# Kernel tuning notes

Hardware: AMD Instinct MI355X
Metric: run time of the kernel (lower is better)

## Reference

```python
import jax, jax.numpy as jnp
import numpy as np

N_NODES = 100000
N_EDGES = 2400000


def setup_inputs() -> dict:
    key = jax.random.key(0)
    ks = jax.random.split(key, 8)
    x = jax.random.normal(ks[0], (N_NODES, 1), dtype=jnp.float32)
    edge_index = jax.random.randint(ks[1], (2, N_EDGES), 0, N_NODES, dtype=jnp.int64)
    # GCNConv weights: lin (in, out) and bias (out,), glorot-ish init
    def w(k, fan_in, fan_out):
        return jax.random.normal(k, (fan_in, fan_out), dtype=jnp.float32) / np.sqrt(fan_in)
    return {
        "x": x,
        "edge_index": edge_index,
        "W1": w(ks[2], 1, 32), "b1": jnp.zeros((32,), jnp.float32),
        "W2": w(ks[3], 32, 16), "b2": jnp.zeros((16,), jnp.float32),
        "W3": w(ks[4], 16, 1), "b3": jnp.zeros((1,), jnp.float32),
    }


def _gcn_conv(x, W, b, src, dst, norm, n):
    # x: [N, Fin] -> linear first (cheaper), then gather-scale-scatter
    h = x @ W                                   # [N, Fout]
    msg = h[src] * norm[:, None]                # [E+N, Fout] gather on src
    out = jax.ops.segment_sum(msg, dst, num_segments=n)  # scatter-add on dst
    return out + b


def reference(x, edge_index, W1, b1, W2, b2, W3, b3):
    n = x.shape[0]
    loops = jnp.arange(n, dtype=edge_index.dtype)
    src = jnp.concatenate([edge_index[0], loops])  # PyG: add self-loops
    dst = jnp.concatenate([edge_index[1], loops])
    # symmetric normalization: deg computed on targets with unit edge weights
    deg = jax.ops.segment_sum(jnp.ones_like(src, dtype=x.dtype), dst, num_segments=n)
    dis = jnp.where(deg > 0, jax.lax.rsqrt(deg), 0.0)
    norm = dis[src] * dis[dst]                  # [E+N]
    h = jax.nn.relu(_gcn_conv(x, W1, b1, src, dst, norm, n))
    h = jax.nn.relu(_gcn_conv(h, W2, b2, src, dst, norm, n))
    return _gcn_conv(h, W3, b3, src, dst, norm, n)
```

## Files before the change

kernel.cpp:

```cpp
#include <hip/hip_runtime.h>
#include <hip/hip_fp16.h>

static constexpr int NN   = 100000;
static constexpr int NE   = 2400000;
static constexpr int BSH  = 7;
static constexpr int BSZ  = 128;
static constexpr int NB   = (NN + BSZ - 1) / BSZ;
static constexpr int MSH  = 9;
static constexpr unsigned MMSK = 511;
static constexpr int MBN  = (NN + 511) / 512;
static constexpr int CAPM = 13184;
static constexpr int NPB  = 512;
static constexpr int SEG  = 4688;
static constexpr int CAP  = 4224;
static_assert((size_t)NPB * SEG >= NE, "segments cover edge list");
static_assert(MBN <= 256, "mid hist fits one pass");
static_assert(NN % 16 == 0, "16-lane-per-node kernels assume NN % 16 == 0");

__global__ __launch_bounds__(256) void khistM(const int* __restrict__ dst,
                                              unsigned* __restrict__ H) {
    __shared__ unsigned h[MBN];
    int b = blockIdx.x, t = threadIdx.x;
    for (int k = t; k < MBN; k += 256) h[k] = 0;
    __syncthreads();
    int off = b * SEG;
    int n = NE - off; if (n > SEG) n = SEG;
    for (int j = t; j < n; j += 256)
        atomicAdd(&h[(unsigned)dst[off + j] >> MSH], 1u);
    __syncthreads();
    for (int k = t; k < MBN; k += 256) H[(size_t)b * MBN + k] = h[k];
}

__global__ __launch_bounds__(512) void kscanM(const unsigned* __restrict__ H,
                                              unsigned* __restrict__ P,
                                              unsigned* __restrict__ cntM) {
    __shared__ unsigned a[512], b2[512];
    int k = blockIdx.x, t = threadIdx.x;
    unsigned v = H[(size_t)t * MBN + k];
    a[t] = v;
    __syncthreads();
    unsigned* cu = a; unsigned* nx = b2;
    for (int o = 1; o < 512; o <<= 1) {
        unsigned x = cu[t];
        if (t >= o) x += cu[t - o];
        nx[t] = x;
        __syncthreads();
        unsigned* tm = cu; cu = nx; nx = tm;
    }
    P[(size_t)k * NPB + t] = cu[t] - v;
    if (t == 511) cntM[k] = cu[t];
}

__global__ __launch_bounds__(256) void kscatterM(const int* __restrict__ src,
                                                 const int* __restrict__ dst,
                                                 const unsigned* __restrict__ P,
                                                 unsigned* __restrict__ csr) {
    __shared__ unsigned lcur[MBN];
    int b = blockIdx.x, t = threadIdx.x;
    for (int k = t; k < MBN; k += 256)
        lcur[k] = (unsigned)k * CAPM + P[(size_t)k * NPB + b];
    __syncthreads();
    int off = b * SEG;
    int n = NE - off; if (n > SEG) n = SEG;
    for (int j = t; j < n; j += 256) {
        unsigned d = (unsigned)dst[off + j], s = (unsigned)src[off + j];
        unsigned pos = atomicAdd(&lcur[d >> MSH], 1u);
        csr[pos] = (s << MSH) | (d & MMSK);
    }
}

__global__ __launch_bounds__(256) void kcsrB(const unsigned* __restrict__ csr,
                                             const unsigned* __restrict__ cntM,
                                             const float* __restrict__ x,
                                             unsigned* __restrict__ csr2,
                                             unsigned* __restrict__ rstart,
                                             unsigned* __restrict__ rcnt,
                                             float* __restrict__ dis,
                                             float* __restrict__ y1) {
    __shared__ unsigned codes[CAP];
    __shared__ unsigned sorted[CAP];
    __shared__ int cnt[BSZ];
    __shared__ int sa[BSZ], sb2[BSZ];
    __shared__ unsigned cur[BSZ];
    __shared__ unsigned top;
    int f = blockIdx.x, t = threadIdx.x;
    unsigned m = (unsigned)f >> 2, fl = (unsigned)f & 3;
    unsigned sbase = m * (unsigned)CAPM;
    unsigned nM = cntM[m]; if (nM > CAPM) nM = CAPM;
    if (t < BSZ) cnt[t] = 0;
    if (t == 0) top = 0;
    __syncthreads();
    for (unsigned j = t; j < nM; j += 256) {
        unsigned c = csr[sbase + j];
        unsigned loc = c & MMSK;
        if ((loc >> BSH) == fl) {
            atomicAdd(&cnt[loc & (BSZ - 1)], 1);
            unsigned p = atomicAdd(&top, 1u);
            if (p < CAP) codes[p] = c;
        }
    }
    __syncthreads();
    unsigned n = top; if (n > CAP) n = CAP;
    if (t < BSZ) sa[t] = cnt[t];
    __syncthreads();
    int* cp = sa; int* xs = sb2;
    for (int o = 1; o < BSZ; o <<= 1) {
        if (t < BSZ) { int v = cp[t]; if (t >= o) v += cp[t - o]; xs[t] = v; }
        __syncthreads();
        int* tm = cp; cp = xs; xs = tm;
    }
    unsigned s0 = (unsigned)f * CAP;
    int node = f * BSZ + t;
    if (t < BSZ) {
        int excl = cp[t] - cnt[t];
        cur[t] = (unsigned)excl;
        if (node < NN) {
            rstart[node] = s0 + (unsigned)excl;
            rcnt[node] = (unsigned)cnt[t];
            float d = rsqrtf((float)(cnt[t] + 1));
            dis[node] = d;
            y1[node] = d * x[node];
        }
    }
    __syncthreads();
    for (unsigned j = t; j < n; j += 256) {
        unsigned cc = codes[j];
        unsigned pos = atomicAdd(&cur[cc & (BSZ - 1)], 1u);
        sorted[pos] = cc >> MSH;
    }
    __syncthreads();
    for (unsigned j = t; j < n; j += 256) csr2[s0 + j] = sorted[j];
}


__global__ __launch_bounds__(256) void kagg1lin(const unsigned* __restrict__ srcs,
                                                const unsigned* __restrict__ rstart,
                                                const unsigned* __restrict__ rcnt,
                                                const float* __restrict__ y1,
                                                const float* __restrict__ dis,
                                                const float* __restrict__ W1,
                                                const float* __restrict__ b1,
                                                const float* __restrict__ W2,
                                                __half* __restrict__ y2) {
    __shared__ float sW1[32], sb1[32], sW2[512];
    int t = threadIdx.x;
    if (t < 32) { sW1[t] = W1[t]; sb1[t] = b1[t]; }
    for (int i = t; i < 512; i += 256) sW2[i] = W2[i];
    __syncthreads();
    int node = blockIdx.x * 16 + (t >> 4);
    int g = t & 15;
    unsigned r0 = rstart[node], r1 = r0 + rcnt[node];
    float s0 = 0.f, s1 = 0.f;
    unsigned j = r0 + g;
    for (; j + 16 < r1; j += 32) {
        unsigned i0 = srcs[j], i1 = srcs[j + 16];
        float v0 = y1[i0], v1 = y1[i1];
        s0 += v0; s1 += v1;
    }
    if (j < r1) s0 += y1[srcs[j]];
    float sum = s0 + s1;
    sum += __shfl_xor(sum, 1, 16);
    sum += __shfl_xor(sum, 2, 16);
    sum += __shfl_xor(sum, 4, 16);
    sum += __shfl_xor(sum, 8, 16);
    float d = dis[node];
    float a = d * (sum + y1[node]);
    float acc = 0.f;
#pragma unroll
    for (int f = 0; f < 32; ++f) {
        float h = fmaxf(a * sW1[f] + sb1[f], 0.f);
        acc += h * sW2[f * 16 + g];
    }
    y2[(size_t)node * 16 + g] = __float2half(d * acc);
}

__global__ __launch_bounds__(256) void kagg16g(const unsigned* __restrict__ srcs,
                                               const unsigned* __restrict__ rstart,
                                               const unsigned* __restrict__ rcnt,
                                               const __half* __restrict__ y2,
                                               const float* __restrict__ dis,
                                               const float* __restrict__ b2,
                                               const float* __restrict__ W3,
                                               float* __restrict__ y3) {
    int t = threadIdx.x;
    int node = blockIdx.x * 16 + (t >> 4);
    int g = t & 15;
    unsigned r0 = rstart[node], r1 = r0 + rcnt[node];
    const __half* yg = y2 + g;
    float s0 = 0.f, s1 = 0.f, s2 = 0.f, s3 = 0.f;
    unsigned j = r0;
    for (; j + 8 <= r1; j += 8) {
        unsigned i0 = srcs[j + 0], i1 = srcs[j + 1], i2 = srcs[j + 2], i3 = srcs[j + 3];
        unsigned i4 = srcs[j + 4], i5 = srcs[j + 5], i6 = srcs[j + 6], i7 = srcs[j + 7];
        float v0 = __half2float(yg[(size_t)i0 * 16]);
        float v1 = __half2float(yg[(size_t)i1 * 16]);
        float v2 = __half2float(yg[(size_t)i2 * 16]);
        float v3 = __half2float(yg[(size_t)i3 * 16]);
        float v4 = __half2float(yg[(size_t)i4 * 16]);
        float v5 = __half2float(yg[(size_t)i5 * 16]);
        float v6 = __half2float(yg[(size_t)i6 * 16]);
        float v7 = __half2float(yg[(size_t)i7 * 16]);
        s0 += v0; s1 += v1; s2 += v2; s3 += v3;
        s0 += v4; s1 += v5; s2 += v6; s3 += v7;
    }
    for (; j + 2 <= r1; j += 2) {
        unsigned i0 = srcs[j], i1 = srcs[j + 1];
        s0 += __half2float(yg[(size_t)i0 * 16]);
        s1 += __half2float(yg[(size_t)i1 * 16]);
    }
    if (j < r1) s2 += __half2float(yg[(size_t)srcs[j] * 16]);
    float sum = (s0 + s1) + (s2 + s3);
    float d = dis[node];
    float a2 = d * (sum + __half2float(y2[(size_t)node * 16 + g])) + b2[g];
    float hg = fmaxf(a2, 0.f) * W3[g];
    hg += __shfl_xor(hg, 1, 16);
    hg += __shfl_xor(hg, 2, 16);
    hg += __shfl_xor(hg, 4, 16);
    hg += __shfl_xor(hg, 8, 16);
    if (g == 0) y3[node] = d * hg;
}

__global__ __launch_bounds__(256) void kaggsg(const unsigned* __restrict__ srcs,
                                              const unsigned* __restrict__ rstart,
                                              const unsigned* __restrict__ rcnt,
                                              const float* __restrict__ y,
                                              const float* __restrict__ dis,
                                              float* __restrict__ out,
                                              const float* __restrict__ bias) {
    int t = threadIdx.x;
    int node = blockIdx.x * 16 + (t >> 4);
    int g = t & 15;
    unsigned r0 = rstart[node], r1 = r0 + rcnt[node];
    float s0 = 0.f, s1 = 0.f;
    unsigned j = r0 + g;
    for (; j + 16 < r1; j += 32) {
        unsigned i0 = srcs[j], i1 = srcs[j + 16];
        float v0 = y[i0], v1 = y[i1];
        s0 += v0; s1 += v1;
    }
    if (j < r1) s0 += y[srcs[j]];
    float sum = s0 + s1;
    sum += __shfl_xor(sum, 1, 16);
    sum += __shfl_xor(sum, 2, 16);
    sum += __shfl_xor(sum, 4, 16);
    sum += __shfl_xor(sum, 8, 16);
    if (g == 0) {
        float d = dis[node];
        out[node] = d * (sum + y[node]) + (bias ? bias[0] : 0.f);
    }
}

extern "C" void kernel_launch(void* const* d_in, const int* in_sizes, int n_in,
                              void* d_out, int out_size, void* d_ws, size_t ws_size,
                              hipStream_t stream) {
    const float* x  = (const float*)d_in[0];
    const int*   ei = (const int*)d_in[1];
    const int* src = ei;
    const int* dst = ei + NE;
    const float* W1 = (const float*)d_in[2];
    const float* b1 = (const float*)d_in[3];
    const float* W2 = (const float*)d_in[4];
    const float* b2 = (const float*)d_in[5];
    const float* W3 = (const float*)d_in[6];
    const float* b3 = (const float*)d_in[7];
    float* out = (float*)d_out;

    auto align256 = [](size_t v) { return (v + 255) & ~(size_t)255; };
    char* w = (char*)d_ws;
    auto carve = [&](size_t bytes) { char* p = w; w += align256(bytes); return p; };

    size_t regA_sz = (size_t)MBN * CAPM * 4;
    char* regA = carve(regA_sz);
    unsigned* csr = (unsigned*)regA;
    __half*   y2  = (__half*)regA;
    unsigned* csr2   = (unsigned*)carve((size_t)NB * CAP * 4);
    unsigned* H      = (unsigned*)carve((size_t)NPB * MBN * 4);
    unsigned* P      = (unsigned*)carve((size_t)MBN * NPB * 4);
    unsigned* cntM   = (unsigned*)carve((size_t)MBN * 4);
    unsigned* rstart = (unsigned*)carve((size_t)NN * 4);
    unsigned* rcnt   = (unsigned*)carve((size_t)NN * 4);
    float*    dis    = (float*)   carve((size_t)NN * 4);
    float*    y1     = (float*)   carve((size_t)NN * 4);
    float*    y3     = (float*)   carve((size_t)NN * 4);

    dim3 B(256);

    khistM   <<<NPB, B, 0, stream>>>(dst, H);
    kscanM   <<<MBN, dim3(512), 0, stream>>>(H, P, cntM);
    kscatterM<<<NPB, B, 0, stream>>>(src, dst, P, csr);
    kcsrB    <<<NB, B, 0, stream>>>(csr, cntM, x, csr2, rstart, rcnt, dis, y1);

    kagg1lin<<<NN / 16, B, 0, stream>>>(csr2, rstart, rcnt, y1, dis, W1, b1, W2, y2);

    kagg16g <<<NN / 16, B, 0, stream>>>(csr2, rstart, rcnt, y2, dis, b2, W3, y3);

    kaggsg  <<<NN / 16, B, 0, stream>>>(csr2, rstart, rcnt, y3, dis, out, b3);
}
```

Baseline: 112.4 us.

## Sort each 512-node mid bucket in one block instead of four filtered passes

The second-level CSR sort now uses one block per 512-node mid bucket instead of four blocks that each re-read the whole bucket and kept only a quarter of the edges. Each block counts all 512 local destinations in shared memory, scans the counts and scatters sources straight to global csr2 without a shared-memory sorted staging buffer. This removes the fourfold redundant reads of each bucket, but launches only 196 blocks with about 53KB of shared memory each, which may leave many CUs idle. The scatter kernel is also unrolled by two to raise memory-level parallelism.

```diff
diff --git a/kernel.cpp b/kernel.cpp
--- a/kernel.cpp
+++ b/kernel.cpp
@@ -3,16 +3,13 @@
 
 static constexpr int NN   = 100000;
 static constexpr int NE   = 2400000;
-static constexpr int BSH  = 7;
-static constexpr int BSZ  = 128;
-static constexpr int NB   = (NN + BSZ - 1) / BSZ;
 static constexpr int MSH  = 9;
 static constexpr unsigned MMSK = 511;
+static constexpr int NND  = 512;
 static constexpr int MBN  = (NN + 511) / 512;
 static constexpr int CAPM = 13184;
 static constexpr int NPB  = 512;
 static constexpr int SEG  = 4688;
-static constexpr int CAP  = 4224;
 static_assert((size_t)NPB * SEG >= NE, "segments cover edge list");
 static_assert(MBN <= 256, "mid hist fits one pass");
 static_assert(NN % 16 == 0, "16-lane-per-node kernels assume NN % 16 == 0");
@@ -62,74 +59,81 @@
     __syncthreads();
     int off = b * SEG;
     int n = NE - off; if (n > SEG) n = SEG;
-    for (int j = t; j < n; j += 256) {
+    int j = t;
+    for (; j + 256 < n; j += 512) {
+        unsigned d0 = (unsigned)dst[off + j],       s0 = (unsigned)src[off + j];
+        unsigned d1 = (unsigned)dst[off + j + 256], s1 = (unsigned)src[off + j + 256];
+        unsigned p0 = atomicAdd(&lcur[d0 >> MSH], 1u);
+        csr[p0] = (s0 << MSH) | (d0 & MMSK);
+        unsigned p1 = atomicAdd(&lcur[d1 >> MSH], 1u);
+        csr[p1] = (s1 << MSH) | (d1 & MMSK);
+    }
+    if (j < n) {
         unsigned d = (unsigned)dst[off + j], s = (unsigned)src[off + j];
         unsigned pos = atomicAdd(&lcur[d >> MSH], 1u);
         csr[pos] = (s << MSH) | (d & MMSK);
     }
 }
 
-__global__ __launch_bounds__(256) void kcsrB(const unsigned* __restrict__ csr,
-                                             const unsigned* __restrict__ cntM,
-                                             const float* __restrict__ x,
-                                             unsigned* __restrict__ csr2,
-                                             unsigned* __restrict__ rstart,
-                                             unsigned* __restrict__ rcnt,
-                                             float* __restrict__ dis,
-                                             float* __restrict__ y1) {
-    __shared__ unsigned codes[CAP];
-    __shared__ unsigned sorted[CAP];
-    __shared__ int cnt[BSZ];
-    __shared__ int sa[BSZ], sb2[BSZ];
-    __shared__ unsigned cur[BSZ];
-    __shared__ unsigned top;
-    int f = blockIdx.x, t = threadIdx.x;
-    unsigned m = (unsigned)f >> 2, fl = (unsigned)f & 3;
-    unsigned sbase = m * (unsigned)CAPM;
+__global__ __launch_bounds__(256) void kcsrB2(const unsigned* __restrict__ csr,
+                                              const unsigned* __restrict__ cntM,
+                                              const float* __restrict__ x,
+                                              unsigned* __restrict__ csr2,
+                                              unsigned* __restrict__ rstart,
+                                              unsigned* __restrict__ rcnt,
+                                              float* __restrict__ dis,
+                                              float* __restrict__ y1) {
+    __shared__ unsigned codes[CAPM];
+    __shared__ int cnt[NND];
+    __shared__ unsigned exs[NND];
+    __shared__ unsigned ps1[256], ps2[256];
+    __shared__ unsigned cur[NND];
+    int m = blockIdx.x, t = threadIdx.x;
+    unsigned sbase = (unsigned)m * CAPM;
     unsigned nM = cntM[m]; if (nM > CAPM) nM = CAPM;
-    if (t < BSZ) cnt[t] = 0;
-    if (t == 0) top = 0;
+    cnt[t] = 0; cnt[t + 256] = 0;
     __syncthreads();
     for (unsigned j = t; j < nM; j += 256) {
         unsigned c = csr[sbase + j];
-        unsigned loc = c & MMSK;
-        if ((loc >> BSH) == fl) {
-            atomicAdd(&cnt[loc & (BSZ - 1)], 1);
-            unsigned p = atomicAdd(&top, 1u);
-            if (p < CAP) codes[p] = c;
-        }
-    }
-    __syncthreads();
-    unsigned n = top; if (n > CAP) n = CAP;
-    if (t < BSZ) sa[t] = cnt[t];
-    __syncthreads();
-    int* cp = sa; int* xs = sb2;
-    for (int o = 1; o < BSZ; o <<= 1) {
-        if (t < BSZ) { int v = cp[t]; if (t >= o) v += cp[t - o]; xs[t] = v; }
+        codes[j] = c;
+        atomicAdd(&cnt[c & MMSK], 1);
+    }
+    __syncthreads();
+    unsigned a0 = (unsigned)cnt[2 * t], a1 = (unsigned)cnt[2 * t + 1];
+    ps1[t] = a0 + a1;
+    __syncthreads();
+    unsigned* cu = ps1; unsigned* nx = ps2;
+    for (int o = 1; o < 256; o <<= 1) {
+        unsigned v = cu[t];
+        if (t >= o) v += cu[t - o];
+        nx[t] = v;
         __syncthreads();
-        int* tm = cp; cp = xs; xs = tm;
-    }
-    unsigned s0 = (unsigned)f * CAP;
-    int node = f * BSZ + t;
-    if (t < BSZ) {
-        int excl = cp[t] - cnt[t];
-        cur[t] = (unsigned)excl;
+        unsigned* tm = cu; cu = nx; nx = tm;
+    }
+    unsigned pexcl = cu[t] - (a0 + a1);
+    exs[2 * t]     = pexcl;
+    exs[2 * t + 1] = pexcl + a0;
+    cur[2 * t]     = pexcl;
+    cur[2 * t + 1] = pexcl + a0;
+#pragma unroll
+    for (int q = 0; q < 2; ++q) {
+        int l = t + q * 256;
+        int node = m * NND + l;
         if (node < NN) {
-            rstart[node] = s0 + (unsigned)excl;
-            rcnt[node] = (unsigned)cnt[t];
-            float d = rsqrtf((float)(cnt[t] + 1));
+            int c = cnt[l];
+            rstart[node] = sbase + exs[l];
+            rcnt[node] = (unsigned)c;
+            float d = rsqrtf((float)(c + 1));
             dis[node] = d;
             y1[node] = d * x[node];
         }
     }
     __syncthreads();
-    for (unsigned j = t; j < n; j += 256) {
-        unsigned cc = codes[j];
-        unsigned pos = atomicAdd(&cur[cc & (BSZ - 1)], 1u);
-        sorted[pos] = cc >> MSH;
-    }
-    __syncthreads();
-    for (unsigned j = t; j < n; j += 256) csr2[s0 + j] = sorted[j];
+    for (unsigned j = t; j < nM; j += 256) {
+        unsigned c = codes[j];
+        unsigned pos = atomicAdd(&cur[c & MMSK], 1u);
+        csr2[sbase + pos] = c >> MSH;
+    }
 }
 
 
@@ -269,11 +273,10 @@
     char* w = (char*)d_ws;
     auto carve = [&](size_t bytes) { char* p = w; w += align256(bytes); return p; };
 
-    size_t regA_sz = (size_t)MBN * CAPM * 4;
-    char* regA = carve(regA_sz);
+    char* regA = carve((size_t)MBN * CAPM * 4);
     unsigned* csr = (unsigned*)regA;
     __half*   y2  = (__half*)regA;
-    unsigned* csr2   = (unsigned*)carve((size_t)NB * CAP * 4);
+    unsigned* csr2   = (unsigned*)carve((size_t)MBN * CAPM * 4);
     unsigned* H      = (unsigned*)carve((size_t)NPB * MBN * 4);
     unsigned* P      = (unsigned*)carve((size_t)MBN * NPB * 4);
     unsigned* cntM   = (unsigned*)carve((size_t)MBN * 4);
@@ -288,7 +291,7 @@
     khistM   <<<NPB, B, 0, stream>>>(dst, H);
     kscanM   <<<MBN, dim3(512), 0, stream>>>(H, P, cntM);
     kscatterM<<<NPB, B, 0, stream>>>(src, dst, P, csr);
-    kcsrB    <<<NB, B, 0, stream>>>(csr, cntM, x, csr2, rstart, rcnt, dis, y1);
+    kcsrB2   <<<MBN, B, 0, stream>>>(csr, cntM, x, csr2, rstart, rcnt, dis, y1);
 
     kagg1lin<<<NN / 16, B, 0, stream>>>(csr2, rstart, rcnt, y1, dis, W1, b1, W2, y2);
 
```

Result: no change. 113.1 us (+0.6%).
